# Optimization experiments

Hardware: AMD Instinct MI355X
Metric: run time of the kernel (lower is better)

## Reference

```python
import jax, jax.numpy as jnp
import numpy as np

NUM_TAGS = 5

def setup_inputs() -> dict:
    key = jax.random.key(0)
    ks = jax.random.split(key, 8)
    B, N, K, Q = 2, 5, 5, 4
    Ls, Lq, D = 128, 128, 768
    inp = {
        'support_token_embedding': jax.random.normal(ks[0], (B * N * K, Ls, D), jnp.float32),
        'query_token_embedding': jax.random.normal(ks[1], (B * N * Q, Lq, D), jnp.float32),
        'support_mask': jnp.ones((B * N * K, Ls), jnp.float32),
        'query_mask': jnp.ones((B * N * Q, Lq), jnp.float32),
        'support_entity_label': jax.random.normal(ks[2], (B * N * K, Ls, NUM_TAGS), jnp.float32),
        'proj_w': jax.random.normal(ks[3], (D, 4 * D), jnp.float32) * 0.02,
        'proj_b': jnp.zeros((D,), jnp.float32),
        'rel_w1': jax.random.normal(ks[4], (D, 4 * D), jnp.float32) * 0.02,
        'rel_b1': jnp.zeros((D,), jnp.float32),
        'rel_w2': jax.random.normal(ks[5], (1, D), jnp.float32) * 0.02,
        'rel_b2': jnp.zeros((1,), jnp.float32),
        'B': B, 'N': N, 'K': K, 'Q': Q,
    }
    return inp

def _fuse(m1, m2):
    return jnp.concatenate([m1, m2, jnp.abs(m1 - m2), m1 * m2], axis=-1)

def reference(support_token_embedding, query_token_embedding, support_mask, query_mask,
              support_entity_label, proj_w, proj_b, rel_w1, rel_b1, rel_w2, rel_b2,
              B, N, K, Q):
    D = support_token_embedding.shape[-1]
    Lq = query_token_embedding.shape[1]

    # ---- cal_bio: per-(sample,shot) tag prototypes, vectorized ----
    labels = jnp.argmax(support_entity_label, axis=-1)                 # [BNK, Ls]
    onehot = jax.nn.one_hot(labels, NUM_TAGS, dtype=jnp.float32)       # [BNK, Ls, T]
    # tag 0 ('O') is additionally gated by the support mask
    masks = jnp.concatenate([onehot[:, :, :1] * support_mask[:, :, None], onehot[:, :, 1:]], axis=2)
    sums = jnp.einsum('blt,bld->btd', masks, support_token_embedding)  # [BNK, T, D]
    cnt = jnp.sum(masks, axis=1)[:, :, None]                           # [BNK, T, 1]
    proto = jnp.where(cnt > 0, sums / jnp.maximum(cnt, 1.0), 0.0)      # [BNK, T, D]
    proto = proto.reshape(B * N, K, NUM_TAGS, D).mean(axis=1)          # mean over K shots
    proto = proto.reshape(B, N, NUM_TAGS, D)                           # support_BIO

    # ---- expand to all (query, class) pairs: batch = B*N*Q*N ----
    BQ = B * N * Q * N
    support = jnp.broadcast_to(proto[:, None], (B, N * Q, N, NUM_TAGS, D)).reshape(BQ, NUM_TAGS, D)
    query = jnp.broadcast_to(query_token_embedding.reshape(B, N * Q, 1, Lq, D),
                             (B, N * Q, N, Lq, D)).reshape(BQ, Lq, D)
    qmask = jnp.broadcast_to(query_mask.reshape(B, N * Q, 1, Lq),
                             (B, N * Q, N, Lq)).reshape(BQ, Lq, 1)
    smask = jnp.ones((BQ, NUM_TAGS, 1), jnp.float32)

    # ---- CoAttention with additive mask bias + post-softmax mask multiply ----
    att = jnp.einsum('bsd,bqd->bsq', support, query) + smask * jnp.swapaxes(qmask, 1, 2) * 100.0
    support_ = jnp.einsum('bsq,bqd->bsd', jax.nn.softmax(att, axis=2), query) * smask
    query_ = jnp.einsum('bqs,bsd->bqd', jax.nn.softmax(jnp.swapaxes(att, 1, 2), axis=2), support) * qmask

    # ---- fuse + proj + relu ----
    es = jax.nn.relu(_fuse(support, support_) @ proj_w.T + proj_b)     # [BQ, T, D]
    eq = jax.nn.relu(_fuse(query, query_) @ proj_w.T + proj_b)        # [BQ, Lq, D]

    # ---- local aggregation: masked max + mean pooling ----
    eq_agg = jnp.concatenate([jnp.max(eq, axis=1), jnp.sum(eq, axis=1) / jnp.sum(qmask, axis=1)], axis=1)
    es_agg = jnp.concatenate([jnp.max(es, axis=1), jnp.sum(es, axis=1) / jnp.sum(smask, axis=1)], axis=1)

    # ---- relation MLP ----
    cat_seq = jnp.concatenate([eq_agg, es_agg], axis=1)                # [BQ, 4D]
    h = jax.nn.relu(cat_seq @ rel_w1.T + rel_b1)
    logits = h @ rel_w2.T + rel_b2                                     # [BQ, 1]
    return logits.reshape(B * N * Q, N)
```

## Files before the change

kernel.cpp:

```cpp
#include <hip/hip_runtime.h>

typedef unsigned short u16;
typedef __attribute__((ext_vector_type(8))) short short8;
typedef __attribute__((ext_vector_type(4))) float f32x4;

#define B_   2
#define N_   5
#define K_   5
#define Q_   4
#define T_   5
#define D_   768
#define L_   128
#define BN_  (B_*N_)
#define BNK_ (B_*N_*K_)
#define BQ_  (B_*N_*Q_*N_)
#define K4_  (4*D_)
#define KFQ  1536
#define AROWS 144

#define QEMB_N  (40*128*768)
#define PROJW_N (768*3072)

__device__ __forceinline__ float bf2f(u16 u) {
    return __uint_as_float(((unsigned)u) << 16);
}
__device__ __forceinline__ u16 f2bf(float f) {
    unsigned u = __float_as_uint(f);
    return (u16)((u + 0x7fffu + ((u >> 16) & 1u)) >> 16);
}
__device__ __forceinline__ void gl_lds16(const u16* g, u16* l) {
    __builtin_amdgcn_global_load_lds(
        (const __attribute__((address_space(1))) unsigned int*)g,
        (__attribute__((address_space(3))) unsigned int*)l, 16, 0, 0);
}

__global__ void k_convert3(const float* __restrict__ q, const float* __restrict__ pw,
                           const float* __restrict__ rw, u16* __restrict__ qo,
                           u16* __restrict__ po, u16* __restrict__ ro) {
    const long n1 = QEMB_N / 4, n2 = PROJW_N / 4;
    const long total = n1 + 2 * n2;
    for (long i = (long)blockIdx.x * 256 + threadIdx.x; i < total; i += (long)gridDim.x * 256) {
        const float* src; u16* dst; long k;
        if (i < n1)            { src = q;  dst = qo; k = i; }
        else if (i < n1 + n2)  { src = pw; dst = po; k = i - n1; }
        else                   { src = rw; dst = ro; k = i - n1 - n2; }
        float4 v = ((const float4*)src)[k];
        u16 o[4] = {f2bf(v.x), f2bf(v.y), f2bf(v.z), f2bf(v.w)};
        *(uint2*)(dst + k * 4) = *(const uint2*)o;
    }
}

__global__ void k_proto_shot(const float* __restrict__ label, const float* __restrict__ smask,
                             const float* __restrict__ semb, float* __restrict__ proto_shot) {
    int bnk = blockIdx.x;
    int s = blockIdx.y;
    __shared__ int   s_tag[L_];
    __shared__ float s_w[L_];
    __shared__ float s_cnt[T_];
    int tid = threadIdx.x;
    if (tid < L_) {
        const float* lp = label + ((long)bnk * L_ + tid) * T_;
        float best = lp[0]; int bi = 0;
        #pragma unroll
        for (int t = 1; t < T_; ++t) { float v = lp[t]; if (v > best) { best = v; bi = t; } }
        s_tag[tid] = bi;
        s_w[tid]   = (bi == 0) ? smask[(long)bnk * L_ + tid] : 1.0f;
    }
    __syncthreads();
    if (tid < T_) {
        float c = 0.f;
        for (int l = 0; l < L_; ++l) if (s_tag[l] == tid) c += s_w[l];
        s_cnt[tid] = c;
    }
    __syncthreads();
    float acc[T_] = {};
    for (int l = 0; l < L_; ++l) {
        float w = s_w[l]; int tg = s_tag[l];
        float e = semb[((long)bnk * L_ + l) * D_ + tid + s * 256] * w;
        #pragma unroll
        for (int t = 0; t < T_; ++t) acc[t] += (tg == t) ? e : 0.0f;
    }
    int d = tid + s * 256;
    #pragma unroll
    for (int t = 0; t < T_; ++t) {
        float c = s_cnt[t];
        float v = (c > 0.f) ? acc[t] / fmaxf(c, 1.f) : 0.f;
        proto_shot[(bnk * T_ + t) * D_ + d] = v;
    }
}

__global__ void k_proto_mean(const float* __restrict__ proto_shot,
                             float* __restrict__ proto_f32, u16* __restrict__ proto_bf) {
    int idx = blockIdx.x * 256 + threadIdx.x;
    if (idx >= BN_ * T_ * D_) return;
    int bn = idx / (T_ * D_);
    int rem = idx - bn * (T_ * D_);
    float s = 0.f;
    #pragma unroll
    for (int k = 0; k < K_; ++k) s += proto_shot[(bn * K_ + k) * (T_ * D_) + rem];
    s *= (1.f / K_);
    proto_f32[idx] = s;
    proto_bf[idx]  = f2bf(s);
}

__global__ void k_attn(const float* __restrict__ qemb, const float* __restrict__ qmask_g,
                       const float* __restrict__ proto_f32,
                       u16* __restrict__ qf, u16* __restrict__ sup_ws,
                       float* __restrict__ p2m_ws, float* __restrict__ qssum_ws) {
    int x = blockIdx.x;
    int xcd = x & 7, slot = x >> 3;
    int g = (slot / 5) * 8 + xcd;
    int n2 = slot % 5;
    int bq = g * 5 + n2;
    int q_idx = g;
    int bn = (bq / (N_ * Q_ * N_)) * N_ + (bq % N_);
    __shared__ float s_proto[T_ * D_];
    __shared__ float s_att[T_][L_];
    __shared__ float s_ps[T_][L_];
    __shared__ float s_p2[L_][8];
    __shared__ float s_qm[L_];
    __shared__ float s_m2[L_][33];
    int tid = threadIdx.x;
    for (int i = tid; i < T_ * D_; i += 256) s_proto[i] = proto_f32[bn * T_ * D_ + i];
    if (tid < L_) s_qm[tid] = qmask_g[(long)q_idx * L_ + tid];
    __syncthreads();
    for (int p = tid; p < T_ * L_; p += 256) {
        int t = p >> 7, q = p & (L_ - 1);
        const float* pp = s_proto + t * D_;
        const float4* qp = (const float4*)(qemb + ((size_t)q_idx * L_ + q) * D_);
        float acc = 0.f;
        #pragma unroll 4
        for (int d = 0; d < D_ / 4; ++d) {
            float4 v = qp[d];
            acc += v.x * pp[4 * d] + v.y * pp[4 * d + 1] + v.z * pp[4 * d + 2] + v.w * pp[4 * d + 3];
        }
        s_att[t][q] = acc + 100.f * s_qm[q];
    }
    __syncthreads();
    if (tid < T_) {
        int t = tid; float m = -1e30f;
        for (int q = 0; q < L_; ++q) m = fmaxf(m, s_att[t][q]);
        float ss = 0.f;
        for (int q = 0; q < L_; ++q) { float e = __expf(s_att[t][q] - m); s_ps[t][q] = e; ss += e; }
        float inv = 1.f / ss;
        for (int q = 0; q < L_; ++q) s_ps[t][q] *= inv;
    } else if (tid >= 128) {
        int q = tid - 128; float m = -1e30f;
        float e[T_];
        #pragma unroll
        for (int t = 0; t < T_; ++t) m = fmaxf(m, s_att[t][q]);
        float ss = 0.f;
        #pragma unroll
        for (int t = 0; t < T_; ++t) { e[t] = __expf(s_att[t][q] - m); ss += e[t]; }
        float inv = s_qm[q] / ss;
        #pragma unroll
        for (int t = 0; t < T_; ++t) {
            s_p2[q][t] = e[t] * inv;
            p2m_ws[((size_t)bq * T_ + t) * L_ + q] = e[t] * inv;
        }
    } else if (tid == 5) {
        float s = 0.f;
        for (int q = 0; q < L_; ++q) s += s_qm[q];
        qssum_ws[bq] = s;
    }
    __syncthreads();
    u16* qfb = qf + (size_t)bq * AROWS * KFQ;
    {
        float acc[T_][3] = {};
        #pragma unroll 4
        for (int q = 0; q < L_; ++q) {
            const float* qp = qemb + ((size_t)q_idx * L_ + q) * D_;
            float qv[3];
            #pragma unroll
            for (int s = 0; s < 3; ++s) qv[s] = qp[tid + s * 256];
            #pragma unroll
            for (int t = 0; t < T_; ++t) {
                float p = s_ps[t][q];
                #pragma unroll
                for (int s = 0; s < 3; ++s) acc[t][s] += p * qv[s];
            }
        }
        #pragma unroll
        for (int t = 0; t < T_; ++t) {
            u16* er = qfb + (size_t)(128 + t) * KFQ;
            #pragma unroll
            for (int s = 0; s < 3; ++s) {
                int d = tid + s * 256;
                float p = s_proto[t * D_ + d];
                float sv = acc[t][s];
                sup_ws[((size_t)bq * T_ + t) * D_ + d] = f2bf(sv);
                er[d]       = f2bf(fabsf(p - sv));
                er[768 + d] = f2bf(p * sv);
            }
        }
    }
    {
        int row_b = tid & 127, half = tid >> 7;
        float pr[T_];
        #pragma unroll
        for (int t = 0; t < T_; ++t) pr[t] = s_p2[row_b][t];
        int d2 = tid & 31, r0 = tid >> 5;
        for (int slab = 0; slab < 24; ++slab) {
            #pragma unroll
            for (int j = 0; j < 16; ++j) {
                int col = half * 16 + j;
                int d = slab * 32 + col;
                float m2 = pr[0] * s_proto[d] + pr[1] * s_proto[D_ + d]
                         + pr[2] * s_proto[2 * D_ + d] + pr[3] * s_proto[3 * D_ + d]
                         + pr[4] * s_proto[4 * D_ + d];
                s_m2[row_b][col] = m2;
            }
            __syncthreads();
            #pragma unroll
            for (int k = 0; k < 16; ++k) {
                int row = r0 + k * 8;
                int dd = slab * 32 + d2;
                float m2 = s_m2[row][d2];
                float qv = qemb[((size_t)q_idx * L_ + row) * D_ + dd];
                u16* qr = qfb + (size_t)row * KFQ;
                qr[dd]        = f2bf(fabsf(qv - m2));
                qr[768 + dd]  = f2bf(qv * m2);
            }
            __syncthreads();
        }
    }
    {
        u16* pr2 = qfb + (size_t)133 * KFQ;
        short8 z = short8{0, 0, 0, 0, 0, 0, 0, 0};
        for (int i = tid; i < (11 * KFQ) / 8; i += 256) *(short8*)(pr2 + i * 8) = z;
    }
}

#define SWZ(g, r) (((g) << 4) + ((r) ^ ((g) << 2)))
__global__ __launch_bounds__(256) void k_gemm_g1(const u16* __restrict__ qemb_bf,
                                                 const u16* __restrict__ proto_bf,
                                                 const u16* __restrict__ projw_bf,
                                                 u16* __restrict__ g1) {
    int mbase = blockIdx.y * 128;
    int jbase = blockIdx.x * 128;
    __shared__ __align__(16) u16 sA[8 * 512];
    __shared__ __align__(16) u16 sB[8 * 512];
    int tid = threadIdx.x;
    int lane = tid & 63, w = tid >> 6, quad = lane >> 4, l16 = lane & 15;
    f32x4 zero = {0.f, 0.f, 0.f, 0.f};
    f32x4 acc[8][2];
    #pragma unroll
    for (int rt = 0; rt < 8; ++rt) { acc[rt][0] = zero; acc[rt][1] = zero; }

    for (int kt = 0; kt < 24; ++kt) {
        int k0 = kt * 32;
        __syncthreads();
        #pragma unroll
        for (int j = 0; j < 2; ++j) {
            int v = tid + j * 256, row = v >> 2, g = v & 3;
            *(uint4*)(sB + (((row >> 4) << 6) + SWZ(g, row & 15)) * 8) =
                *(const uint4*)(projw_bf + (size_t)(jbase + row) * K4_ + k0 + g * 8);
            int grow = mbase + row;
            uint4 av = uint4{0u, 0u, 0u, 0u};
            if (grow < 5120)      av = *(const uint4*)(qemb_bf + (size_t)grow * D_ + k0 + g * 8);
            else if (grow < 5170) av = *(const uint4*)(proto_bf + (size_t)(grow - 5120) * D_ + k0 + g * 8);
            *(uint4*)(sA + (((row >> 4) << 6) + SWZ(g, row & 15)) * 8) = av;
        }
        __syncthreads();
        short8 af[8], bfr[2];
        #pragma unroll
        for (int rt = 0; rt < 8; ++rt)
            af[rt] = *(const short8*)(sA + ((rt << 6) + SWZ(quad, l16)) * 8);
        #pragma unroll
        for (int jj = 0; jj < 2; ++jj)
            bfr[jj] = *(const short8*)(sB + (((w * 2 + jj) << 6) + SWZ(quad, l16)) * 8);
        #pragma unroll
        for (int rt = 0; rt < 8; ++rt)
            #pragma unroll
            for (int jj = 0; jj < 2; ++jj)
                acc[rt][jj] = __builtin_amdgcn_mfma_f32_16x16x32_bf16(af[rt], bfr[jj], acc[rt][jj], 0, 0, 0);
    }
    #pragma unroll
    for (int jj = 0; jj < 2; ++jj) {
        int col = jbase + (w * 2 + jj) * 16 + l16;
        #pragma unroll
        for (int rt = 0; rt < 8; ++rt)
            #pragma unroll
            for (int r = 0; r < 4; ++r) {
                int row = mbase + rt * 16 + quad * 4 + r;
                g1[(size_t)row * D_ + col] = f2bf(acc[rt][jj][r]);
            }
    }
}

__global__ __launch_bounds__(256) void k_gemm_w2(const u16* __restrict__ sup_ws,
                                                 const u16* __restrict__ proto_bf,
                                                 const u16* __restrict__ projw_bf,
                                                 u16* __restrict__ sw2, u16* __restrict__ pw2) {
    int mbase = blockIdx.y * 128;
    int jbase = blockIdx.x * 128;
    __shared__ __align__(16) u16 sA[8 * 512];
    __shared__ __align__(16) u16 sB[8 * 512];
    int tid = threadIdx.x;
    int lane = tid & 63, w = tid >> 6, quad = lane >> 4, l16 = lane & 15;
    f32x4 zero = {0.f, 0.f, 0.f, 0.f};
    f32x4 acc[8][2];
    #pragma unroll
    for (int rt = 0; rt < 8; ++rt) { acc[rt][0] = zero; acc[rt][1] = zero; }

    for (int kt = 0; kt < 24; ++kt) {
        int k0 = kt * 32;
        __syncthreads();
        #pragma unroll
        for (int j = 0; j < 2; ++j) {
            int v = tid + j * 256, row = v >> 2, g = v & 3;
            *(uint4*)(sB + (((row >> 4) << 6) + SWZ(g, row & 15)) * 8) =
                *(const uint4*)(projw_bf + (size_t)(jbase + row) * K4_ + 768 + k0 + g * 8);
            int grow = mbase + row;
            uint4 av = uint4{0u, 0u, 0u, 0u};
            if (grow < 1000)      av = *(const uint4*)(sup_ws + (size_t)grow * D_ + k0 + g * 8);
            else if (grow < 1050) av = *(const uint4*)(proto_bf + (size_t)(grow - 1000) * D_ + k0 + g * 8);
            *(uint4*)(sA + (((row >> 4) << 6) + SWZ(g, row & 15)) * 8) = av;
        }
        __syncthreads();
        short8 af[8], bfr[2];
        #pragma unroll
        for (int rt = 0; rt < 8; ++rt)
            af[rt] = *(const short8*)(sA + ((rt << 6) + SWZ(quad, l16)) * 8);
        #pragma unroll
        for (int jj = 0; jj < 2; ++jj)
            bfr[jj] = *(const short8*)(sB + (((w * 2 + jj) << 6) + SWZ(quad, l16)) * 8);
        #pragma unroll
        for (int rt = 0; rt < 8; ++rt)
            #pragma unroll
            for (int jj = 0; jj < 2; ++jj)
                acc[rt][jj] = __builtin_amdgcn_mfma_f32_16x16x32_bf16(af[rt], bfr[jj], acc[rt][jj], 0, 0, 0);
    }
    #pragma unroll
    for (int jj = 0; jj < 2; ++jj) {
        int col = jbase + (w * 2 + jj) * 16 + l16;
        #pragma unroll
        for (int rt = 0; rt < 8; ++rt)
            #pragma unroll
            for (int r = 0; r < 4; ++r) {
                int row = mbase + rt * 16 + quad * 4 + r;
                if (row < 1000)      sw2[(size_t)row * D_ + col] = f2bf(acc[rt][jj][r]);
                else if (row < 1050) pw2[(size_t)(row - 1000) * D_ + col] = f2bf(acc[rt][jj][r]);
            }
    }
}

#define SUBSZ ((AROWS + 128) * 32)
__global__ __launch_bounds__(256) void k_gemm_q(
        const u16* __restrict__ qf, const u16* __restrict__ projw_bf,
        const float* __restrict__ projb, const u16* __restrict__ g1,
        const u16* __restrict__ pw2, const u16* __restrict__ sw2,
        const float* __restrict__ p2m, const float* __restrict__ qssum_ws,
        u16* __restrict__ cat_ws) {
    int x = blockIdx.x;
    int xcd = x & 7, slot = x >> 3;
    int i = slot / 6, jslot = slot % 6;
    int g = (i / 5) * 8 + xcd;
    int bq = g * 5 + (i % 5);
    int jbase = jslot * 128;
    int q_idx = bq / N_;
    int bn = (bq / (N_ * Q_ * N_)) * N_ + (bq % N_);
    __shared__ __align__(16) u16 sT[2][2 * SUBSZ];
    __shared__ float s_p2mL[T_ * 128];
    __shared__ float s_pw2L[T_ * 128];
    int tid = threadIdx.x;
    int lane = tid & 63, w = tid >> 6, quad = lane >> 4, l16 = lane & 15;
    int srow = lane >> 2, sko = lane & 3;
    const u16* Ab = qf + ((size_t)bq * AROWS + srow) * KFQ + sko * 8;
    const u16* Bb = projw_bf + (size_t)(jbase + srow) * K4_ + 1536 + sko * 8;

    f32x4 zero = {0.f, 0.f, 0.f, 0.f};
    f32x4 acc[9][2];
    #pragma unroll
    for (int rt = 0; rt < 9; ++rt) { acc[rt][0] = zero; acc[rt][1] = zero; }

    auto issue = [&](int kt, int b) {
        #pragma unroll
        for (int s = 0; s < 2; ++s) {
            int k0 = kt * 64 + s * 32;
            u16* base = sT[b] + s * SUBSZ;
            gl_lds16(Ab + (size_t)(w * 16) * KFQ + k0, base + (w * 16) * 32);
            gl_lds16(Ab + (size_t)(64 + w * 16) * KFQ + k0, base + (64 + w * 16) * 32);
            if (w == 0) gl_lds16(Ab + (size_t)128 * KFQ + k0, base + 128 * 32);
            gl_lds16(Bb + (size_t)(w * 16) * K4_ + k0, base + (AROWS + w * 16) * 32);
            gl_lds16(Bb + (size_t)(64 + w * 16) * K4_ + k0, base + (AROWS + 64 + w * 16) * 32);
        }
    };

    issue(0, 0);
    for (int kt = 0; kt < KFQ / 64; ++kt) {
        int cur = kt & 1;
        __syncthreads();
        if (kt + 1 < KFQ / 64) issue(kt + 1, 1 - cur);
        #pragma unroll
        for (int s = 0; s < 2; ++s) {
            const u16* base = sT[cur] + s * SUBSZ;
            short8 bfr[2];
            #pragma unroll
            for (int jj = 0; jj < 2; ++jj)
                bfr[jj] = *(const short8*)(base + (AROWS + (w * 2 + jj) * 16 + l16) * 32 + quad * 8);
            #pragma unroll
            for (int rt = 0; rt < 9; ++rt) {
                short8 a = *(const short8*)(base + (rt * 16 + l16) * 32 + quad * 8);
                acc[rt][0] = __builtin_amdgcn_mfma_f32_16x16x32_bf16(a, bfr[0], acc[rt][0], 0, 0, 0);
                acc[rt][1] = __builtin_amdgcn_mfma_f32_16x16x32_bf16(a, bfr[1], acc[rt][1], 0, 0, 0);
            }
        }
    }
    for (int i2 = tid; i2 < T_ * 128; i2 += 256) {
        s_p2mL[i2] = p2m[(size_t)bq * (T_ * 128) + i2];
        s_pw2L[i2] = bf2f(pw2[(size_t)(bn * T_ + (i2 >> 7)) * D_ + jbase + (i2 & 127)]);
    }
    __syncthreads();
    float inv_qs = 1.f / qssum_ws[bq];
    #pragma unroll
    for (int jj = 0; jj < 2; ++jj) {
        int col = jbase + (w * 2 + jj) * 16 + l16;
        int cj = (w * 2 + jj) * 16 + l16;
        float bias = projb[col];
        float qmax = 0.f, qsum = 0.f, smax = 0.f, ssum = 0.f;
        #pragma unroll
        for (int rt = 0; rt < 8; ++rt) {
            #pragma unroll
            for (int r = 0; r < 4; ++r) {
                int row = rt * 16 + quad * 4 + r;
                float g1v = bf2f(g1[(size_t)(q_idx * 128 + row) * D_ + col]);
                float mix = s_p2mL[row] * s_pw2L[cj]
                          + s_p2mL[128 + row] * s_pw2L[128 + cj]
                          + s_p2mL[256 + row] * s_pw2L[256 + cj]
                          + s_p2mL[384 + row] * s_pw2L[384 + cj]
                          + s_p2mL[512 + row] * s_pw2L[512 + cj];
                float v = fmaxf(acc[rt][jj][r] + g1v + mix + bias, 0.f);
                qmax = fmaxf(qmax, v); qsum += v;
            }
        }
        #pragma unroll
        for (int r = 0; r < 4; ++r) {
            int t = quad * 4 + r;
            if (t < T_) {
                float g1v = bf2f(g1[(size_t)(5120 + bn * T_ + t) * D_ + col]);
                float s2v = bf2f(sw2[(size_t)(bq * T_ + t) * D_ + col]);
                float v = fmaxf(acc[8][jj][r] + g1v + s2v + bias, 0.f);
                smax = fmaxf(smax, v); ssum += v;
            }
        }
        qmax = fmaxf(qmax, __shfl_xor(qmax, 16, 64)); qmax = fmaxf(qmax, __shfl_xor(qmax, 32, 64));
        qsum += __shfl_xor(qsum, 16, 64);             qsum += __shfl_xor(qsum, 32, 64);
        smax = fmaxf(smax, __shfl_xor(smax, 16, 64)); smax = fmaxf(smax, __shfl_xor(smax, 32, 64));
        ssum += __shfl_xor(ssum, 16, 64);             ssum += __shfl_xor(ssum, 32, 64);
        if (quad == 0) {
            u16* cp = cat_ws + (size_t)bq * K4_;
            cp[col]           = f2bf(qmax);
            cp[D_ + col]      = f2bf(qsum * inv_qs);
            cp[2 * D_ + col]  = f2bf(smax);
            cp[3 * D_ + col]  = f2bf(ssum * 0.2f);
        }
    }
}

#define AST  40
__global__ __launch_bounds__(256) void k_relmlp(const u16* __restrict__ cat_ws,
                                                const u16* __restrict__ w1,
                                                float* __restrict__ part) {
    int mbase = blockIdx.y * 64;
    int jbase = blockIdx.x * 128;
    int ks = blockIdx.z;
    __shared__ __align__(16) u16 sA[64 * AST];
    __shared__ __align__(16) u16 sB[128 * AST];
    int tid = threadIdx.x;
    int lane = tid & 63, w = tid >> 6, quad = lane >> 4, l16 = lane & 15;
    f32x4 zero = {0.f, 0.f, 0.f, 0.f};
    f32x4 acc[4][2];
    #pragma unroll
    for (int rt = 0; rt < 4; ++rt) { acc[rt][0] = zero; acc[rt][1] = zero; }

    for (int kt = ks * 12; kt < ks * 12 + 12; ++kt) {
        int k0 = kt * 32;
        __syncthreads();
        {
            int row = tid >> 2, ko = (tid & 3) * 8;
            int grow = mbase + row;
            short8 val = short8{0, 0, 0, 0, 0, 0, 0, 0};
            if (grow < BQ_) val = *(const short8*)(cat_ws + (size_t)grow * K4_ + k0 + ko);
            *(short8*)(sA + row * AST + ko) = val;
        }
        for (int u = tid; u < 512; u += 256) {
            int row = u >> 2, ko = (u & 3) * 8;
            *(short8*)(sB + row * AST + ko) =
                *(const short8*)(w1 + (size_t)(jbase + row) * K4_ + k0 + ko);
        }
        __syncthreads();
        short8 af[4], bfr[2];
        #pragma unroll
        for (int rt = 0; rt < 4; ++rt)
            af[rt] = *(const short8*)(sA + (rt * 16 + l16) * AST + quad * 8);
        #pragma unroll
        for (int jj = 0; jj < 2; ++jj)
            bfr[jj] = *(const short8*)(sB + ((2 * w + jj) * 16 + l16) * AST + quad * 8);
        #pragma unroll
        for (int rt = 0; rt < 4; ++rt)
            #pragma unroll
            for (int jj = 0; jj < 2; ++jj)
                acc[rt][jj] = __builtin_amdgcn_mfma_f32_16x16x32_bf16(af[rt], bfr[jj], acc[rt][jj], 0, 0, 0);
    }
    #pragma unroll
    for (int jj = 0; jj < 2; ++jj) {
        int col = jbase + (2 * w + jj) * 16 + l16;
        #pragma unroll
        for (int rt = 0; rt < 4; ++rt) {
            #pragma unroll
            for (int r = 0; r < 4; ++r) {
                int grow = mbase + rt * 16 + quad * 4 + r;
                if (grow < BQ_)
                    part[((size_t)ks * BQ_ + grow) * D_ + col] = acc[rt][jj][r];
            }
        }
    }
}

__global__ void k_rel_fin(const float* __restrict__ part, const float* __restrict__ b1,
                          const float* __restrict__ w2, const float* __restrict__ b2,
                          float* __restrict__ out) {
    int bq = blockIdx.x, tid = threadIdx.x;
    float a = 0.f;
    #pragma unroll
    for (int s = 0; s < 3; ++s) {
        int col = tid + s * 256;
        float sum = 0.f;
        #pragma unroll
        for (int ks = 0; ks < 8; ++ks) sum += part[((size_t)ks * BQ_ + bq) * D_ + col];
        float h = fmaxf(sum + b1[col], 0.f);
        a += h * w2[col];
    }
    __shared__ float red[256];
    red[tid] = a; __syncthreads();
    for (int off = 128; off >= 1; off >>= 1) {
        if (tid < off) red[tid] += red[tid + off];
        __syncthreads();
    }
    if (tid == 0) out[bq] = red[0] + b2[0];
}

extern "C" void kernel_launch(void* const* d_in, const int* in_sizes, int n_in,
                              void* d_out, int out_size, void* d_ws, size_t ws_size,
                              hipStream_t stream) {
    (void)in_sizes; (void)n_in; (void)out_size; (void)ws_size;
    const float* semb  = (const float*)d_in[0];
    const float* qemb  = (const float*)d_in[1];
    const float* smask = (const float*)d_in[2];
    const float* qmask = (const float*)d_in[3];
    const float* label = (const float*)d_in[4];
    const float* projw = (const float*)d_in[5];
    const float* projb = (const float*)d_in[6];
    const float* relw1 = (const float*)d_in[7];
    const float* relb1 = (const float*)d_in[8];
    const float* relw2 = (const float*)d_in[9];
    const float* relb2 = (const float*)d_in[10];

    char* ws = (char*)d_ws;
    u16*   qemb_bf   = (u16*)  (ws + 0);
    u16*   projw_bf  = (u16*)  (ws + 7864320);
    u16*   relw1_bf  = (u16*)  (ws + 12582912);
    float* proto_shot= (float*)(ws + 17301504);
    float* proto_f32 = (float*)(ws + 18069504);
    u16*   proto_bf  = (u16*)  (ws + 18223104);
    float* qssum     = (float*)(ws + 18299904);
    u16*   sup_ws    = (u16*)  (ws + 18300800);
    float* p2m_ws    = (float*)(ws + 19836800);
    u16*   pw2_ws    = (u16*)  (ws + 20348800);
    u16*   sw2_ws    = (u16*)  (ws + 20425600);
    u16*   cat_ws    = (u16*)  (ws + 21961600);
    u16*   g1_ws     = (u16*)  (ws + 23190400);
    float* part_ws   = (float*)(ws + 31251328);
    u16*   qf_ws     = (u16*)  (ws + 36166528);

    k_convert3<<<2048, 256, 0, stream>>>(qemb, projw, relw1, qemb_bf, projw_bf, relw1_bf);
    k_proto_shot<<<dim3(BNK_, 3), 256, 0, stream>>>(label, smask, semb, proto_shot);
    k_proto_mean<<<150, 256, 0, stream>>>(proto_shot, proto_f32, proto_bf);
    k_attn<<<BQ_, 256, 0, stream>>>(qemb, qmask, proto_f32, qf_ws, sup_ws, p2m_ws, qssum);
    k_gemm_g1<<<dim3(6, 41), 256, 0, stream>>>(qemb_bf, proto_bf, projw_bf, g1_ws);
    k_gemm_w2<<<dim3(6, 9), 256, 0, stream>>>(sup_ws, proto_bf, projw_bf, sw2_ws, pw2_ws);
    k_gemm_q<<<1200, 256, 0, stream>>>(qf_ws, projw_bf, projb, g1_ws, pw2_ws, sw2_ws,
                                       p2m_ws, qssum, cat_ws);
    k_relmlp<<<dim3(6, 4, 8), 256, 0, stream>>>(cat_ws, relw1_bf, part_ws);
    k_rel_fin<<<BQ_, 256, 0, stream>>>(part_ws, relb1, relw2, relb2, (float*)d_out);
}
```

Baseline: 507.7 us.

## Merge g1 and w2 GEMMs into one padded A matrix with async LDS double buffering

Builds a single contiguous bf16 A matrix holding query embeddings, prototypes, support vectors and a second prototype copy, with padding rows zeroed in the proto-mean kernel. The two projection GEMMs are replaced by one kernel that picks the projw column offset per row block and stages tiles through double-buffered global-to-LDS loads. This drops a launch, removes per-row bounds branches in the loaders and lets loads overlap MFMA work. k_attn's qf build also drops its shared-memory staging and slab barriers and computes m2 per wave directly. The trade-offs are extra zero-fill writes and LDS reads without the earlier swizzle, which may cause bank conflicts.

```diff
diff --git a/kernel.cpp b/kernel.cpp
--- a/kernel.cpp
+++ b/kernel.cpp
@@ -20,6 +20,10 @@
 
 #define QEMB_N  (40*128*768)
 #define PROJW_N (768*3072)
+#define R_PROTO1 5120
+#define R_SUP    5248
+#define R_PROTO2 6248
+#define R_TOTAL  6400
 
 __device__ __forceinline__ float bf2f(u16 u) {
     return __uint_as_float(((unsigned)u) << 16);
@@ -90,22 +94,35 @@
 }
 
 __global__ void k_proto_mean(const float* __restrict__ proto_shot,
-                             float* __restrict__ proto_f32, u16* __restrict__ proto_bf) {
-    int idx = blockIdx.x * 256 + threadIdx.x;
-    if (idx >= BN_ * T_ * D_) return;
-    int bn = idx / (T_ * D_);
-    int rem = idx - bn * (T_ * D_);
-    float s = 0.f;
-    #pragma unroll
-    for (int k = 0; k < K_; ++k) s += proto_shot[(bn * K_ + k) * (T_ * D_) + rem];
-    s *= (1.f / K_);
-    proto_f32[idx] = s;
-    proto_bf[idx]  = f2bf(s);
+                             float* __restrict__ proto_f32, u16* __restrict__ A_all) {
+    int bx = blockIdx.x;
+    if (bx < 150) {
+        int idx = bx * 256 + threadIdx.x;
+        if (idx >= BN_ * T_ * D_) return;
+        int r = idx / D_, d = idx - r * D_;
+        int bn = r / T_;
+        int rem = idx - bn * (T_ * D_);
+        float s = 0.f;
+        #pragma unroll
+        for (int k = 0; k < K_; ++k) s += proto_shot[(bn * K_ + k) * (T_ * D_) + rem];
+        s *= (1.f / K_);
+        proto_f32[idx] = s;
+        u16 b = f2bf(s);
+        A_all[(size_t)(R_PROTO1 + r) * D_ + d] = b;
+        A_all[(size_t)(R_PROTO2 + r) * D_ + d] = b;
+    } else {
+        int zidx = (bx - 150) * 256 + threadIdx.x;
+        if (zidx >= 59904 + 78336) return;
+        size_t off;
+        if (zidx < 59904) off = (size_t)5170 * D_ + zidx;
+        else              off = (size_t)6298 * D_ + (zidx - 59904);
+        A_all[off] = 0;
+    }
 }
 
 __global__ void k_attn(const float* __restrict__ qemb, const float* __restrict__ qmask_g,
                        const float* __restrict__ proto_f32,
-                       u16* __restrict__ qf, u16* __restrict__ sup_ws,
+                       u16* __restrict__ qf, u16* __restrict__ supA,
                        float* __restrict__ p2m_ws, float* __restrict__ qssum_ws) {
     int x = blockIdx.x;
     int xcd = x & 7, slot = x >> 3;
@@ -119,8 +136,8 @@
     __shared__ float s_ps[T_][L_];
     __shared__ float s_p2[L_][8];
     __shared__ float s_qm[L_];
-    __shared__ float s_m2[L_][33];
     int tid = threadIdx.x;
+    int w = tid >> 6, lane = tid & 63;
     for (int i = tid; i < T_ * D_; i += 256) s_proto[i] = proto_f32[bn * T_ * D_ + i];
     if (tid < L_) s_qm[tid] = qmask_g[(long)q_idx * L_ + tid];
     __syncthreads();
@@ -188,40 +205,26 @@
                 int d = tid + s * 256;
                 float p = s_proto[t * D_ + d];
                 float sv = acc[t][s];
-                sup_ws[((size_t)bq * T_ + t) * D_ + d] = f2bf(sv);
+                supA[((size_t)bq * T_ + t) * D_ + d] = f2bf(sv);
                 er[d]       = f2bf(fabsf(p - sv));
                 er[768 + d] = f2bf(p * sv);
             }
         }
     }
-    {
-        int row_b = tid & 127, half = tid >> 7;
-        float pr[T_];
-        #pragma unroll
-        for (int t = 0; t < T_; ++t) pr[t] = s_p2[row_b][t];
-        int d2 = tid & 31, r0 = tid >> 5;
-        for (int slab = 0; slab < 24; ++slab) {
-            #pragma unroll
-            for (int j = 0; j < 16; ++j) {
-                int col = half * 16 + j;
-                int d = slab * 32 + col;
-                float m2 = pr[0] * s_proto[d] + pr[1] * s_proto[D_ + d]
-                         + pr[2] * s_proto[2 * D_ + d] + pr[3] * s_proto[3 * D_ + d]
-                         + pr[4] * s_proto[4 * D_ + d];
-                s_m2[row_b][col] = m2;
-            }
-            __syncthreads();
-            #pragma unroll
-            for (int k = 0; k < 16; ++k) {
-                int row = r0 + k * 8;
-                int dd = slab * 32 + d2;
-                float m2 = s_m2[row][d2];
-                float qv = qemb[((size_t)q_idx * L_ + row) * D_ + dd];
-                u16* qr = qfb + (size_t)row * KFQ;
-                qr[dd]        = f2bf(fabsf(qv - m2));
-                qr[768 + dd]  = f2bf(qv * m2);
-            }
-            __syncthreads();
+    for (int rr = 0; rr < 32; ++rr) {
+        int row = w * 32 + rr;
+        float p0 = s_p2[row][0], p1 = s_p2[row][1], p2v = s_p2[row][2];
+        float p3 = s_p2[row][3], p4 = s_p2[row][4];
+        const float* qrow = qemb + ((size_t)q_idx * L_ + row) * D_;
+        u16* qr = qfb + (size_t)row * KFQ;
+        #pragma unroll
+        for (int ch = 0; ch < 12; ++ch) {
+            int c = ch * 64 + lane;
+            float m2 = p0 * s_proto[c] + p1 * s_proto[D_ + c] + p2v * s_proto[2 * D_ + c]
+                     + p3 * s_proto[3 * D_ + c] + p4 * s_proto[4 * D_ + c];
+            float qv = qrow[c];
+            qr[c]       = f2bf(fabsf(qv - m2));
+            qr[768 + c] = f2bf(qv * m2);
         }
     }
     {
@@ -231,49 +234,57 @@
     }
 }
 
-#define SWZ(g, r) (((g) << 4) + ((r) ^ ((g) << 2)))
-__global__ __launch_bounds__(256) void k_gemm_g1(const u16* __restrict__ qemb_bf,
-                                                 const u16* __restrict__ proto_bf,
+#define SUBGW ((128 + 128) * 32)
+__global__ __launch_bounds__(256) void k_gemm_gw(const u16* __restrict__ A_all,
                                                  const u16* __restrict__ projw_bf,
-                                                 u16* __restrict__ g1) {
+                                                 u16* __restrict__ g1, u16* __restrict__ sw2,
+                                                 u16* __restrict__ pw2) {
     int mbase = blockIdx.y * 128;
     int jbase = blockIdx.x * 128;
-    __shared__ __align__(16) u16 sA[8 * 512];
-    __shared__ __align__(16) u16 sB[8 * 512];
+    int boff = (mbase >= R_SUP) ? 768 : 0;
+    __shared__ __align__(16) u16 sT[2][2 * SUBGW];
     int tid = threadIdx.x;
     int lane = tid & 63, w = tid >> 6, quad = lane >> 4, l16 = lane & 15;
+    int srow = lane >> 2, sko = lane & 3;
+    const u16* Ab = A_all + ((size_t)mbase + srow) * D_ + sko * 8;
+    const u16* Bb = projw_bf + (size_t)(jbase + srow) * K4_ + boff + sko * 8;
+
     f32x4 zero = {0.f, 0.f, 0.f, 0.f};
     f32x4 acc[8][2];
     #pragma unroll
     for (int rt = 0; rt < 8; ++rt) { acc[rt][0] = zero; acc[rt][1] = zero; }
 
-    for (int kt = 0; kt < 24; ++kt) {
-        int k0 = kt * 32;
+    auto issue = [&](int kt, int b) {
+        #pragma unroll
+        for (int s = 0; s < 2; ++s) {
+            int k0 = kt * 64 + s * 32;
+            u16* base = sT[b] + s * SUBGW;
+            gl_lds16(Ab + (size_t)(w * 16) * D_ + k0, base + (w * 16) * 32);
+            gl_lds16(Ab + (size_t)(64 + w * 16) * D_ + k0, base + (64 + w * 16) * 32);
+            gl_lds16(Bb + (size_t)(w * 16) * K4_ + k0, base + (128 + w * 16) * 32);
+            gl_lds16(Bb + (size_t)(64 + w * 16) * K4_ + k0, base + (128 + 64 + w * 16) * 32);
+        }
+    };
+
+    issue(0, 0);
+    for (int kt = 0; kt < D_ / 64; ++kt) {
+        int cur = kt & 1;
         __syncthreads();
-        #pragma unroll
-        for (int j = 0; j < 2; ++j) {
-            int v = tid + j * 256, row = v >> 2, g = v & 3;
-            *(uint4*)(sB + (((row >> 4) << 6) + SWZ(g, row & 15)) * 8) =
-                *(const uint4*)(projw_bf + (size_t)(jbase + row) * K4_ + k0 + g * 8);
-            int grow = mbase + row;
-            uint4 av = uint4{0u, 0u, 0u, 0u};
-            if (grow < 5120)      av = *(const uint4*)(qemb_bf + (size_t)grow * D_ + k0 + g * 8);
-            else if (grow < 5170) av = *(const uint4*)(proto_bf + (size_t)(grow - 5120) * D_ + k0 + g * 8);
-            *(uint4*)(sA + (((row >> 4) << 6) + SWZ(g, row & 15)) * 8) = av;
-        }
-        __syncthreads();
-        short8 af[8], bfr[2];
-        #pragma unroll
-        for (int rt = 0; rt < 8; ++rt)
-            af[rt] = *(const short8*)(sA + ((rt << 6) + SWZ(quad, l16)) * 8);
-        #pragma unroll
-        for (int jj = 0; jj < 2; ++jj)
-            bfr[jj] = *(const short8*)(sB + (((w * 2 + jj) << 6) + SWZ(quad, l16)) * 8);
-        #pragma unroll
-        for (int rt = 0; rt < 8; ++rt)
+        if (kt + 1 < D_ / 64) issue(kt + 1, 1 - cur);
+        #pragma unroll
+        for (int s = 0; s < 2; ++s) {
+            const u16* base = sT[cur] + s * SUBGW;
+            short8 bfr[2];
             #pragma unroll
             for (int jj = 0; jj < 2; ++jj)
-                acc[rt][jj] = __builtin_amdgcn_mfma_f32_16x16x32_bf16(af[rt], bfr[jj], acc[rt][jj], 0, 0, 0);
+                bfr[jj] = *(const short8*)(base + (128 + (w * 2 + jj) * 16 + l16) * 32 + quad * 8);
+            #pragma unroll
+            for (int rt = 0; rt < 8; ++rt) {
+                short8 a = *(const short8*)(base + (rt * 16 + l16) * 32 + quad * 8);
+                acc[rt][0] = __builtin_amdgcn_mfma_f32_16x16x32_bf16(a, bfr[0], acc[rt][0], 0, 0, 0);
+                acc[rt][1] = __builtin_amdgcn_mfma_f32_16x16x32_bf16(a, bfr[1], acc[rt][1], 0, 0, 0);
+            }
+        }
     }
     #pragma unroll
     for (int jj = 0; jj < 2; ++jj) {
@@ -283,64 +294,10 @@
             #pragma unroll
             for (int r = 0; r < 4; ++r) {
                 int row = mbase + rt * 16 + quad * 4 + r;
-                g1[(size_t)row * D_ + col] = f2bf(acc[rt][jj][r]);
-            }
-    }
-}
-
-__global__ __launch_bounds__(256) void k_gemm_w2(const u16* __restrict__ sup_ws,
-                                                 const u16* __restrict__ proto_bf,
-                                                 const u16* __restrict__ projw_bf,
-                                                 u16* __restrict__ sw2, u16* __restrict__ pw2) {
-    int mbase = blockIdx.y * 128;
-    int jbase = blockIdx.x * 128;
-    __shared__ __align__(16) u16 sA[8 * 512];
-    __shared__ __align__(16) u16 sB[8 * 512];
-    int tid = threadIdx.x;
-    int lane = tid & 63, w = tid >> 6, quad = lane >> 4, l16 = lane & 15;
-    f32x4 zero = {0.f, 0.f, 0.f, 0.f};
-    f32x4 acc[8][2];
-    #pragma unroll
-    for (int rt = 0; rt < 8; ++rt) { acc[rt][0] = zero; acc[rt][1] = zero; }
-
-    for (int kt = 0; kt < 24; ++kt) {
-        int k0 = kt * 32;
-        __syncthreads();
-        #pragma unroll
-        for (int j = 0; j < 2; ++j) {
-            int v = tid + j * 256, row = v >> 2, g = v & 3;
-            *(uint4*)(sB + (((row >> 4) << 6) + SWZ(g, row & 15)) * 8) =
-                *(const uint4*)(projw_bf + (size_t)(jbase + row) * K4_ + 768 + k0 + g * 8);
-            int grow = mbase + row;
-            uint4 av = uint4{0u, 0u, 0u, 0u};
-            if (grow < 1000)      av = *(const uint4*)(sup_ws + (size_t)grow * D_ + k0 + g * 8);
-            else if (grow < 1050) av = *(const uint4*)(proto_bf + (size_t)(grow - 1000) * D_ + k0 + g * 8);
-            *(uint4*)(sA + (((row >> 4) << 6) + SWZ(g, row & 15)) * 8) = av;
-        }
-        __syncthreads();
-        short8 af[8], bfr[2];
-        #pragma unroll
-        for (int rt = 0; rt < 8; ++rt)
-            af[rt] = *(const short8*)(sA + ((rt << 6) + SWZ(quad, l16)) * 8);
-        #pragma unroll
-        for (int jj = 0; jj < 2; ++jj)
-            bfr[jj] = *(const short8*)(sB + (((w * 2 + jj) << 6) + SWZ(quad, l16)) * 8);
-        #pragma unroll
-        for (int rt = 0; rt < 8; ++rt)
-            #pragma unroll
-            for (int jj = 0; jj < 2; ++jj)
-                acc[rt][jj] = __builtin_amdgcn_mfma_f32_16x16x32_bf16(af[rt], bfr[jj], acc[rt][jj], 0, 0, 0);
-    }
-    #pragma unroll
-    for (int jj = 0; jj < 2; ++jj) {
-        int col = jbase + (w * 2 + jj) * 16 + l16;
-        #pragma unroll
-        for (int rt = 0; rt < 8; ++rt)
-            #pragma unroll
-            for (int r = 0; r < 4; ++r) {
-                int row = mbase + rt * 16 + quad * 4 + r;
-                if (row < 1000)      sw2[(size_t)row * D_ + col] = f2bf(acc[rt][jj][r]);
-                else if (row < 1050) pw2[(size_t)(row - 1000) * D_ + col] = f2bf(acc[rt][jj][r]);
+                u16 v = f2bf(acc[rt][jj][r]);
+                if (row < R_SUP)            g1[(size_t)row * D_ + col] = v;
+                else if (row < R_PROTO2)    sw2[(size_t)(row - R_SUP) * D_ + col] = v;
+                else if (row < R_PROTO2+50) pw2[(size_t)(row - R_PROTO2) * D_ + col] = v;
             }
     }
 }
@@ -558,28 +515,26 @@
     const float* relb2 = (const float*)d_in[10];
 
     char* ws = (char*)d_ws;
-    u16*   qemb_bf   = (u16*)  (ws + 0);
-    u16*   projw_bf  = (u16*)  (ws + 7864320);
-    u16*   relw1_bf  = (u16*)  (ws + 12582912);
-    float* proto_shot= (float*)(ws + 17301504);
-    float* proto_f32 = (float*)(ws + 18069504);
-    u16*   proto_bf  = (u16*)  (ws + 18223104);
-    float* qssum     = (float*)(ws + 18299904);
-    u16*   sup_ws    = (u16*)  (ws + 18300800);
-    float* p2m_ws    = (float*)(ws + 19836800);
-    u16*   pw2_ws    = (u16*)  (ws + 20348800);
-    u16*   sw2_ws    = (u16*)  (ws + 20425600);
-    u16*   cat_ws    = (u16*)  (ws + 21961600);
-    u16*   g1_ws     = (u16*)  (ws + 23190400);
-    float* part_ws   = (float*)(ws + 31251328);
-    u16*   qf_ws     = (u16*)  (ws + 36166528);
-
-    k_convert3<<<2048, 256, 0, stream>>>(qemb, projw, relw1, qemb_bf, projw_bf, relw1_bf);
+    u16*   A_all     = (u16*)  (ws + 0);
+    u16*   projw_bf  = (u16*)  (ws + 9830400);
+    u16*   relw1_bf  = (u16*)  (ws + 14548992);
+    float* proto_shot= (float*)(ws + 19267584);
+    float* proto_f32 = (float*)(ws + 20035584);
+    float* qssum     = (float*)(ws + 20189184);
+    float* p2m_ws    = (float*)(ws + 20190080);
+    u16*   pw2_ws    = (u16*)  (ws + 20702080);
+    u16*   sw2_ws    = (u16*)  (ws + 20778880);
+    u16*   cat_ws    = (u16*)  (ws + 22314880);
+    u16*   g1_ws     = (u16*)  (ws + 23543680);
+    float* part_ws   = (float*)(ws + 31604608);
+    u16*   qf_ws     = (u16*)  (ws + 36519808);
+
+    k_convert3<<<2048, 256, 0, stream>>>(qemb, projw, relw1, A_all, projw_bf, relw1_bf);
     k_proto_shot<<<dim3(BNK_, 3), 256, 0, stream>>>(label, smask, semb, proto_shot);
-    k_proto_mean<<<150, 256, 0, stream>>>(proto_shot, proto_f32, proto_bf);
-    k_attn<<<BQ_, 256, 0, stream>>>(qemb, qmask, proto_f32, qf_ws, sup_ws, p2m_ws, qssum);
-    k_gemm_g1<<<dim3(6, 41), 256, 0, stream>>>(qemb_bf, proto_bf, projw_bf, g1_ws);
-    k_gemm_w2<<<dim3(6, 9), 256, 0, stream>>>(sup_ws, proto_bf, projw_bf, sw2_ws, pw2_ws);
+    k_proto_mean<<<691, 256, 0, stream>>>(proto_shot, proto_f32, A_all);
+    k_attn<<<BQ_, 256, 0, stream>>>(qemb, qmask, proto_f32, qf_ws, A_all + (size_t)R_SUP * D_,
+                                    p2m_ws, qssum);
+    k_gemm_gw<<<dim3(6, 50), 256, 0, stream>>>(A_all, projw_bf, g1_ws, sw2_ws, pw2_ws);
     k_gemm_q<<<1200, 256, 0, stream>>>(qf_ws, projw_bf, projb, g1_ws, pw2_ws, sw2_ws,
                                        p2m_ws, qssum, cat_ws);
     k_relmlp<<<dim3(6, 4, 8), 256, 0, stream>>>(cat_ws, relw1_bf, part_ws);
```

New measurement: 463.4 us. 8.7% less time.
